# Optimization experiments

Hardware: AMD Instinct MI355X
Metric: run time of the kernel (lower is better)

Reference implementation:

```python
import jax, jax.numpy as jnp
import numpy as np
import math

B = 8; SEQ = 1000; C_IN = 32; D = 512; H = 8; DK = 64; DV = 64
DFF = 2048; NL = 4; ARY = 4; INNER = 5


def get_mask_np(seq_size, ary, inner):
    # full k-ary tree sizes (padded) and effective sizes per scale
    full = 1
    while full < seq_size:
        full *= ary
    all_size = [full]; effe = [seq_size]
    while all_size[-1] > 1:
        all_size.append(all_size[-1] // ary)
        effe.append(math.ceil(effe[-1] / ary))
    n = sum(all_size)
    allow = np.zeros((n, n), dtype=bool)
    w = inner // 2
    starts = np.concatenate([[0], np.cumsum(all_size)]).astype(int)
    # intra-scale local window
    for l, sz in enumerate(all_size):
        s = starts[l]
        for i in range(sz):
            lo = max(i - w, 0); hi = min(i + w + 1, sz)
            allow[s + i, s + lo:s + hi] = True
    # inter-scale parent<->children links
    for l in range(1, len(all_size)):
        s = starts[l]; ps = starts[l - 1]
        for i in range(all_size[l]):
            lo = ps + i * ary; hi = ps + (i + 1) * ary
            allow[s + i, lo:hi] = True
            allow[lo:hi, s + i] = True
    return allow, all_size, effe

ALLOW_NP, ALL_SIZE, EFFE_SIZE = get_mask_np(SEQ, ARY, INNER)
NTOT = sum(ALL_SIZE)   # 1365
DEPTH = len(ALL_SIZE)  # 6
OFFS = np.concatenate([[0], np.cumsum(ALL_SIZE)]).astype(int)


def sinusoid_pe(length, d):
    pos = np.arange(length)[:, None].astype(np.float64)
    i = np.arange(d)[None, :]
    ang = pos / np.power(10000.0, (2 * (i // 2)) / d)
    pe = np.zeros((length, d), np.float32)
    pe[:, 0::2] = np.sin(ang[:, 0::2]); pe[:, 1::2] = np.cos(ang[:, 1::2])
    return pe

PE_NP = sinusoid_pe(SEQ, D)


def layer_norm(x, s, b, eps=1e-5):
    m = x.mean(-1, keepdims=True)
    v = ((x - m) ** 2).mean(-1, keepdims=True)
    return (x - m) * jax.lax.rsqrt(v + eps) * s + b


def setup_inputs() -> dict:
    key = jax.random.key(0)
    ks = jax.random.split(key, 10)
    p = lambda k, shape, sc=0.02: jax.random.normal(k, shape, jnp.float32) * sc
    return {
        "x": jax.random.normal(ks[0], (B, SEQ, C_IN), jnp.float32),
        "conv_w": p(ks[1], (D, C_IN, 3), 0.05),
        "norm_s": jnp.ones((D,), jnp.float32), "norm_b": jnp.zeros((D,), jnp.float32),
        "wq": p(ks[2], (NL, D, H * DK)), "wk": p(ks[3], (NL, D, H * DK)),
        "wv": p(ks[4], (NL, D, H * DV)), "wo": p(ks[5], (NL, H * DV, D)),
        "ln1_s": jnp.ones((NL, D), jnp.float32), "ln1_b": jnp.zeros((NL, D), jnp.float32),
        "w1": p(ks[6], (NL, D, DFF)), "b1": jnp.zeros((NL, DFF), jnp.float32),
        "w2": p(ks[7], (NL, DFF, D)), "b2": jnp.zeros((NL, D), jnp.float32),
        "ln2_s": jnp.ones((NL, D), jnp.float32), "ln2_b": jnp.zeros((NL, D), jnp.float32),
    }


def reference(x, conv_w, norm_s, norm_b, wq, wk, wv, wo, ln1_s, ln1_b,
              w1, b1, w2, b2, ln2_s, ln2_b):
    allow = jnp.asarray(ALLOW_NP)        # [N,N] True = attend
    pe = jnp.asarray(PE_NP)              # [S,D]
    # --- DataEmbedding: conv1d(k=3, circular pad, no bias) + sinusoid PE ---
    xt = jnp.concatenate([x[:, -1:], x, x[:, :1]], axis=1)       # (B,S+2,C)
    emb = jax.lax.conv_general_dilated(
        xt, conv_w, (1,), 'VALID', dimension_numbers=('NWC', 'OIW', 'NWC'))
    emb = emb + pe[None]                                          # (B,S,D)
    # pad sequence to full-tree leaf count
    emb = jnp.pad(emb, ((0, 0), (0, ALL_SIZE[0] - SEQ), (0, 0)))  # (B,L0,D)
    # --- MaxPooling_Construct: pool by ary per level, concat, LayerNorm ---
    parts = [emb]
    cur = emb
    for lvl in range(DEPTH - 1):
        L = cur.shape[1]
        cur = cur.reshape(B, L // ARY, ARY, D).max(axis=2)
        parts.append(cur)
    seq = jnp.concatenate(parts, axis=1)                          # (B,N,D)
    seq = layer_norm(seq, norm_s, norm_b)
    # --- masked MHA encoder layers (post-norm) ---
    scale = 1.0 / math.sqrt(DK)
    neg = jnp.float32(-1e9)
    for l in range(NL):
        q = (seq @ wq[l]).reshape(B, NTOT, H, DK)
        k = (seq @ wk[l]).reshape(B, NTOT, H, DK)
        v = (seq @ wv[l]).reshape(B, NTOT, H, DV)
        scores = jnp.einsum('bnhd,bmhd->bhnm', q, k) * scale
        scores = jnp.where(allow[None, None], scores, neg)
        attn = jax.nn.softmax(scores, axis=-1)
        ctx = jnp.einsum('bhnm,bmhd->bnhd', attn, v).reshape(B, NTOT, H * DV)
        seq = layer_norm(seq + ctx @ wo[l], ln1_s[l], ln1_b[l])
        ff = jax.nn.gelu(seq @ w1[l] + b1[l], approximate=False) @ w2[l] + b2[l]
        seq = layer_norm(seq + ff, ln2_s[l], ln2_b[l])
    # --- keep only the effective (unpadded) prefix of each scale ---
    out = jnp.concatenate(
        [seq[:, OFFS[i]:OFFS[i] + EFFE_SIZE[i]] for i in range(DEPTH)], axis=1)
    return out  # (B, sum(effe)=1334, D)
```

## Files before the change

### kernel.cpp

```cpp
#include <hip/hip_runtime.h>
#include <cstdint>
#include <math.h>

#define DEV __device__ __forceinline__

static constexpr int BQ = 8, SEQN = 1000, CIN = 32, NH = 8;
static constexpr int NLAY = 4;
static constexpr int NTOT_C = 1365;
static constexpr int M_REAL = BQ * NTOT_C;
static constexpr int M_PAD  = 11008;

DEV float bf2f(unsigned short u){ return __uint_as_float(((unsigned)u) << 16); }
DEV unsigned short f2bf(float f){
  unsigned u = __float_as_uint(f);
  u += 0x7fffu + ((u >> 16) & 1u);
  return (unsigned short)(u >> 16);
}

typedef __bf16 bf16x8 __attribute__((ext_vector_type(8)));
typedef float  f32x4  __attribute__((ext_vector_type(4)));
typedef unsigned short u16x8 __attribute__((ext_vector_type(8)));

#define GLD_LDS16(gp, lp) __builtin_amdgcn_global_load_lds( \
    (const __attribute__((address_space(1))) void*)(gp), \
    (__attribute__((address_space(3))) void*)(lp), 16, 0, 0)

template<int N> DEV void waitcnt_vm(){
  asm volatile("s_waitcnt vmcnt(%0)" :: "i"(N) : "memory");
}
DEV void waitcnt_lgkm0(){ asm volatile("s_waitcnt lgkmcnt(0)" ::: "memory"); }
DEV void cfence(){ asm volatile("" ::: "memory"); }

DEV float gelu_f(float x){
  float z = 0.7978845608028654f * (x + 0.044715f * x * x * x);
  z = fminf(fmaxf(z, -10.f), 10.f);
  float e = __expf(2.f * z);
  float th = (e - 1.f) / (e + 1.f);
  return 0.5f * x * (1.f + th);
}

__global__ __launch_bounds__(256) void pe_kernel(float* __restrict__ pe)
{
  int idx = blockIdx.x * 256 + threadIdx.x;
  int d = idx & 511, s = idx >> 9;
  if (s >= SEQN) return;
  float e2 = (float)(d & ~1);
  float freq = exp2f(e2 * (-13.287712379549449f / 512.0f));
  float ang = (float)s * freq;
  pe[idx] = (d & 1) ? cosf(ang) : sinf(ang);
}

__global__ __launch_bounds__(256) void conv_kernel(const float* __restrict__ x,
    const float* __restrict__ w, const float* __restrict__ pe, float* __restrict__ seqf)
{
  __shared__ float ws_w[128 * 97];
  __shared__ __align__(16) float xs[66][32];
  int b = blockIdx.z, s0 = blockIdx.y * 64, d0 = blockIdx.x * 128;
  int tid = threadIdx.x;
  for (int i = tid; i < 128 * 96; i += 256){
    int r = i / 96, c = i - r * 96;
    ws_w[r * 97 + c] = w[(size_t)(d0 + r) * 96 + c];
  }
  for (int i = tid; i < 66 * 32; i += 256){
    int r = i >> 5, c = i & 31;
    int ss = s0 + r - 1;
    ss = (ss < 0) ? (ss + SEQN) : (ss >= SEQN ? ss - SEQN : ss);
    xs[r][c] = x[((size_t)b * SEQN + ss) * CIN + c];
  }
  __syncthreads();
  int dl = tid & 127, sh = tid >> 7;
  float wr[96];
  #pragma unroll
  for (int i = 0; i < 96; i++) wr[i] = ws_w[dl * 97 + i];
  int d = d0 + dl;
  for (int si = 0; si < 32; si++){
    int sl = sh * 32 + si;
    int s = s0 + sl;
    float acc = 0.f;
    #pragma unroll
    for (int kk = 0; kk < 3; kk++){
      const float* xr = xs[sl + kk];
      #pragma unroll
      for (int c = 0; c < 32; c++) acc += xr[c] * wr[c * 3 + kk];
    }
    float outv = (s < SEQN) ? acc + pe[(size_t)s * 512 + d] : 0.f;
    seqf[((size_t)b * NTOT_C + s) * 512 + d] = outv;
  }
}

__global__ __launch_bounds__(256) void pool_kernel(float* __restrict__ seqf,
    int inOff, int outOff, int outSz)
{
  int e = blockIdx.x * 256 + threadIdx.x;
  int d = e & 511;
  int r = e >> 9;
  int i = r % outSz;
  int b = r / outSz;
  const float* src = seqf + ((size_t)b * NTOT_C + inOff + 4 * i) * 512 + d;
  float m = fmaxf(fmaxf(src[0], src[512]), fmaxf(src[1024], src[1536]));
  seqf[((size_t)b * NTOT_C + outOff + i) * 512 + d] = m;
}

__global__ __launch_bounds__(256) void ln4_kernel(const float* __restrict__ xin,
    float* __restrict__ outf, unsigned short* __restrict__ outb,
    const float* __restrict__ sg, const float* __restrict__ bg, int M)
{
  int row = blockIdx.x * 4 + (threadIdx.x >> 6);
  int lane = threadIdx.x & 63;
  size_t base = (size_t)row * 512 + lane * 8;
  if (row >= M){
    f32x4 z4 = {0.f, 0.f, 0.f, 0.f};
    *reinterpret_cast<f32x4*>(outf + base) = z4;
    *reinterpret_cast<f32x4*>(outf + base + 4) = z4;
    u16x8 z8 = {0, 0, 0, 0, 0, 0, 0, 0};
    *reinterpret_cast<u16x8*>(outb + base) = z8;
    return;
  }
  f32x4 v0 = *reinterpret_cast<const f32x4*>(xin + base);
  f32x4 v1 = *reinterpret_cast<const f32x4*>(xin + base + 4);
  float sall = v0[0] + v0[1] + v0[2] + v0[3] + v1[0] + v1[1] + v1[2] + v1[3];
  #pragma unroll
  for (int o = 32; o; o >>= 1) sall += __shfl_xor(sall, o, 64);
  float mean = sall * (1.f / 512.f);
  float d[8];
  #pragma unroll
  for (int e = 0; e < 4; e++){ d[e] = v0[e] - mean; d[4 + e] = v1[e] - mean; }
  float sq = 0.f;
  #pragma unroll
  for (int e = 0; e < 8; e++) sq += d[e] * d[e];
  #pragma unroll
  for (int o = 32; o; o >>= 1) sq += __shfl_xor(sq, o, 64);
  float rstd = 1.f / sqrtf(sq * (1.f / 512.f) + 1e-5f);
  f32x4 s0 = *reinterpret_cast<const f32x4*>(sg + lane * 8);
  f32x4 s1 = *reinterpret_cast<const f32x4*>(sg + lane * 8 + 4);
  f32x4 g0 = *reinterpret_cast<const f32x4*>(bg + lane * 8);
  f32x4 g1 = *reinterpret_cast<const f32x4*>(bg + lane * 8 + 4);
  f32x4 y0, y1; u16x8 yb;
  #pragma unroll
  for (int e = 0; e < 4; e++){
    y0[e] = d[e] * rstd * s0[e] + g0[e];
    y1[e] = d[4 + e] * rstd * s1[e] + g1[e];
    yb[e] = f2bf(y0[e]); yb[4 + e] = f2bf(y1[e]);
  }
  *reinterpret_cast<f32x4*>(outf + base) = y0;
  *reinterpret_cast<f32x4*>(outf + base + 4) = y1;
  *reinterpret_cast<u16x8*>(outb + base) = yb;
}

__global__ __launch_bounds__(256) void wconv_all(
    const float* __restrict__ wq, const float* __restrict__ wk,
    const float* __restrict__ wv, const float* __restrict__ wo,
    const float* __restrict__ w1, const float* __restrict__ w2,
    unsigned short* __restrict__ qkvT, unsigned short* __restrict__ woT,
    unsigned short* __restrict__ w1T, unsigned short* __restrict__ w2T)
{
  __shared__ float tile[32][33];
  int bid = blockIdx.x;
  const float* wl; unsigned short* wtl; int N, K, n0, k0;
  if (bid < 4096){
    int part = bid >> 10, t = bid & 1023;
    int l = t >> 8, t2 = t & 255;
    k0 = (t2 >> 4) * 32; n0 = (t2 & 15) * 32;
    N = 512; K = 512;
    const float* s = (part == 0) ? wq : (part == 1) ? wk : (part == 2) ? wv : wo;
    wl = s + (size_t)l * 512 * 512;
    wtl = (part < 3) ? (qkvT + (size_t)l * 1536 * 512 + (size_t)part * 512 * 512)
                     : (woT + (size_t)l * 512 * 512);
  } else if (bid < 8192){
    int t = bid - 4096, l = t >> 10, t2 = t & 1023;
    k0 = (t2 >> 6) * 32; n0 = (t2 & 63) * 32;
    N = 2048; K = 512;
    wl = w1 + (size_t)l * 512 * 2048;
    wtl = w1T + (size_t)l * 2048 * 512;
  } else {
    int t = bid - 8192, l = t >> 10, t2 = t & 1023;
    k0 = (t2 >> 4) * 32; n0 = (t2 & 15) * 32;
    N = 512; K = 2048;
    wl = w2 + (size_t)l * 2048 * 512;
    wtl = w2T + (size_t)l * 512 * 2048;
  }
  int c = threadIdx.x & 31, r8 = threadIdx.x >> 5;
  #pragma unroll
  for (int p = 0; p < 4; p++){ int r = r8 + p * 8; tile[r][c] = wl[(size_t)(k0 + r) * N + n0 + c]; }
  __syncthreads();
  #pragma unroll
  for (int p = 0; p < 4; p++){ int r = r8 + p * 8; wtl[(size_t)(n0 + r) * K + k0 + c] = f2bf(tile[c][r]); }
}

template<int EPI, int BM, int BN>
__global__ __launch_bounds__(256) void gemm2_kernel(
    const unsigned short* __restrict__ A, const unsigned short* __restrict__ Wt,
    float* __restrict__ Cf, unsigned short* __restrict__ Cb,
    const float* __restrict__ bias, const float* __restrict__ Rf, int N, int K)
{
  constexpr int MF = BM / 32, NF = BN / 32;
  constexpr int LA = BM / 32, LB = BN / 32;
  __shared__ __align__(16) unsigned short Abuf[2][BM * 64];
  __shared__ __align__(16) unsigned short Bbuf[2][BN * 64];
  const int tid = threadIdx.x;
  const int wid = tid >> 6, lane = tid & 63;
  const int wm2 = wid >> 1, wn2 = wid & 1;
  const int r16 = lane & 15, g = lane >> 4;
  const int m0 = blockIdx.x * BM, n0 = blockIdx.y * BN;

  const int row0 = tid >> 3;
  const int scol = ((tid & 7) ^ (row0 & 7)) * 8;
  const unsigned short* gAs = A  + (size_t)(m0 + row0) * K + scol;
  const unsigned short* gBs = Wt + (size_t)(n0 + row0) * K + scol;

  const int swz0 = ((0 + g) ^ (r16 & 7)) * 8;
  const int swz1 = ((4 + g) ^ (r16 & 7)) * 8;
  const int arow = (wm2 * (BM / 2) + r16) * 64;
  const int brow = (wn2 * (BN / 2) + r16) * 64;

  const int nt = K >> 6;
  f32x4 acc[MF][NF] = {};

  auto STAGE_A = [&](int buf, int kt){
    #pragma unroll
    for (int q = 0; q < LA; q++)
      GLD_LDS16(gAs + kt * 64 + (size_t)q * 32 * K, &Abuf[buf][q * 2048 + tid * 8]);
  };
  auto STAGE_B = [&](int buf, int kt){
    #pragma unroll
    for (int q = 0; q < LB; q++)
      GLD_LDS16(gBs + kt * 64 + (size_t)q * 32 * K, &Bbuf[buf][q * 2048 + tid * 8]);
  };

  cfence();
  STAGE_A(0, 0); STAGE_B(0, 0);
  if (nt > 1){ STAGE_A(1, 1); waitcnt_vm<LA>(); }
  else        { waitcnt_vm<0>(); }
  __builtin_amdgcn_s_barrier();
  cfence();

  for (int t = 0; t < nt; t++){
    const int d = t & 1;
    const unsigned short* Ab = Abuf[d];
    const unsigned short* Bb = Bbuf[d];

    bf16x8 a0[MF], b0[NF];
    #pragma unroll
    for (int m = 0; m < MF; m++) a0[m] = *reinterpret_cast<const bf16x8*>(&Ab[arow + m * 1024 + swz0]);
    #pragma unroll
    for (int n = 0; n < NF; n++) b0[n] = *reinterpret_cast<const bf16x8*>(&Bb[brow + n * 1024 + swz0]);
    if (t + 1 < nt){ cfence(); STAGE_B(d ^ 1, t + 1); cfence(); }
    __builtin_amdgcn_s_setprio(1);
    #pragma unroll
    for (int m = 0; m < MF; m++)
      #pragma unroll
      for (int n = 0; n < NF; n++)
        acc[m][n] = __builtin_amdgcn_mfma_f32_16x16x32_bf16(a0[m], b0[n], acc[m][n], 0, 0, 0);
    __builtin_amdgcn_s_setprio(0);

    bf16x8 a1[MF], b1v[NF];
    #pragma unroll
    for (int m = 0; m < MF; m++) a1[m] = *reinterpret_cast<const bf16x8*>(&Ab[arow + m * 1024 + swz1]);
    #pragma unroll
    for (int n = 0; n < NF; n++) b1v[n] = *reinterpret_cast<const bf16x8*>(&Bb[brow + n * 1024 + swz1]);
    waitcnt_lgkm0();
    __builtin_amdgcn_s_barrier();
    cfence();
    if (t + 2 < nt){ STAGE_A(d, t + 2); cfence(); }
    __builtin_amdgcn_s_setprio(1);
    #pragma unroll
    for (int m = 0; m < MF; m++)
      #pragma unroll
      for (int n = 0; n < NF; n++)
        acc[m][n] = __builtin_amdgcn_mfma_f32_16x16x32_bf16(a1[m], b1v[n], acc[m][n], 0, 0, 0);
    __builtin_amdgcn_s_setprio(0);

    if (t + 1 < nt){
      if (t + 2 < nt) waitcnt_vm<LA>();
      else            waitcnt_vm<0>();
      __builtin_amdgcn_s_barrier();
      cfence();
    }
  }

  const int colBase = n0 + wn2 * (BN / 2) + r16;
  #pragma unroll
  for (int m = 0; m < MF; m++){
    int row = m0 + wm2 * (BM / 2) + m * 16 + g * 4;
    #pragma unroll
    for (int n = 0; n < NF; n++){
      int col = colBase + n * 16;
      float bsv = (EPI >= 2) ? bias[col] : 0.f;
      #pragma unroll
      for (int j = 0; j < 4; j++){
        float v = acc[m][n][j];
        if (EPI >= 2) v += bsv;
        if (EPI == 2) v = gelu_f(v);
        size_t off = (size_t)(row + j) * N + col;
        if (EPI == 0 || EPI == 3) Cf[off] = v + Rf[off];
        else                      Cb[off] = f2bf(v);
      }
    }
  }
}

__global__ __launch_bounds__(256) void attn_kernel(
    const unsigned short* __restrict__ qkv, unsigned short* __restrict__ ctx)
{
  int wid = blockIdx.x * 4 + (threadIdx.x >> 6);
  int lane = threadIdx.x & 63;
  int n = wid % NTOT_C;
  int b = wid / NTOT_C;

  int i, sz, of, cb, par;
  if (n < 1024){ i = n;        sz = 1024; of = 0;    cb = -1;            par = 1024 + (i >> 2); }
  else if (n < 1280){ i = n - 1024; sz = 256; of = 1024; cb = 0    + 4 * i; par = 1280 + (i >> 2); }
  else if (n < 1344){ i = n - 1280; sz = 64;  of = 1280; cb = 1024 + 4 * i; par = 1344 + (i >> 2); }
  else if (n < 1360){ i = n - 1344; sz = 16;  of = 1344; cb = 1280 + 4 * i; par = 1360 + (i >> 2); }
  else if (n < 1364){ i = n - 1360; sz = 4;   of = 1360; cb = 1344 + 4 * i; par = 1364; }
  else { i = 0; sz = 1; of = 1364; cb = 1360; par = -1; }

  int nb[10];
  #pragma unroll
  for (int s5 = 0; s5 < 5; s5++){ int pos = i - 2 + s5; nb[s5] = (pos >= 0 && pos < sz) ? of + pos : -1; }
  #pragma unroll
  for (int r = 0; r < 4; r++) nb[5 + r] = (cb >= 0) ? cb + r : -1;
  nb[9] = par;

  const unsigned short* rows = qkv + ((size_t)b * NTOT_C) * 1536;

  u16x8 qv = *reinterpret_cast<const u16x8*>(rows + (size_t)n * 1536 + lane * 8);
  float qf[8];
  #pragma unroll
  for (int e = 0; e < 8; e++) qf[e] = bf2f(qv[e]);

  float sc[10];
  #pragma unroll
  for (int j = 0; j < 10; j++){
    int id = nb[j] >= 0 ? nb[j] : n;
    u16x8 kv = *reinterpret_cast<const u16x8*>(rows + (size_t)id * 1536 + 512 + lane * 8);
    float p = 0.f;
    #pragma unroll
    for (int e = 0; e < 8; e++) p += qf[e] * bf2f(kv[e]);
    p += __shfl_xor(p, 1, 64);
    p += __shfl_xor(p, 2, 64);
    p += __shfl_xor(p, 4, 64);
    sc[j] = (nb[j] >= 0) ? p * 0.125f : -1e30f;
  }
  float mx = sc[0];
  #pragma unroll
  for (int j = 1; j < 10; j++) mx = fmaxf(mx, sc[j]);
  float den = 0.f;
  float wj[10];
  #pragma unroll
  for (int j = 0; j < 10; j++){
    wj[j] = (nb[j] >= 0) ? expf(sc[j] - mx) : 0.f;
    den += wj[j];
  }
  float rden = 1.f / den;
  float accv[8] = {};
  #pragma unroll
  for (int j = 0; j < 10; j++){
    int id = nb[j] >= 0 ? nb[j] : n;
    u16x8 vv = *reinterpret_cast<const u16x8*>(rows + (size_t)id * 1536 + 1024 + lane * 8);
    float w = wj[j];
    #pragma unroll
    for (int e = 0; e < 8; e++) accv[e] += w * bf2f(vv[e]);
  }
  u16x8 ov;
  #pragma unroll
  for (int e = 0; e < 8; e++) ov[e] = f2bf(accv[e] * rden);
  *reinterpret_cast<u16x8*>(ctx + ((size_t)b * NTOT_C + n) * 512 + lane * 8) = ov;
}

__global__ __launch_bounds__(256) void gather_kernel(const float* __restrict__ seqf,
    float* __restrict__ out)
{
  int e = blockIdx.x * 256 + threadIdx.x;
  int d = e & 511;
  int r = e >> 9;
  int j = r % 1334;
  int b = r / 1334;
  int src;
  if      (j < 1000) src = j;
  else if (j < 1250) src = j + 24;
  else if (j < 1313) src = j + 30;
  else if (j < 1333) src = j + 31;
  else               src = 1364;
  out[e] = seqf[((size_t)b * NTOT_C + src) * 512 + d];
}

extern "C" void kernel_launch(void* const* d_in, const int* in_sizes, int n_in,
                              void* d_out, int out_size, void* d_ws, size_t ws_size,
                              hipStream_t stream)
{
  const float* x      = (const float*)d_in[0];
  const float* conv_w = (const float*)d_in[1];
  const float* norm_s = (const float*)d_in[2];
  const float* norm_b = (const float*)d_in[3];
  const float* wq     = (const float*)d_in[4];
  const float* wk     = (const float*)d_in[5];
  const float* wv     = (const float*)d_in[6];
  const float* wo     = (const float*)d_in[7];
  const float* ln1_s  = (const float*)d_in[8];
  const float* ln1_b  = (const float*)d_in[9];
  const float* w1     = (const float*)d_in[10];
  const float* b1     = (const float*)d_in[11];
  const float* w2     = (const float*)d_in[12];
  const float* b2     = (const float*)d_in[13];
  const float* ln2_s  = (const float*)d_in[14];
  const float* ln2_b  = (const float*)d_in[15];
  float* out = (float*)d_out;

  char* ws = (char*)d_ws;
  size_t off = 0;
  auto alloc = [&](size_t bytes) -> char* {
    char* p = ws + off; off += (bytes + 255) & ~(size_t)255; return p;
  };
  unsigned short* qkvT = (unsigned short*)alloc((size_t)NLAY * 1536 * 512 * 2);
  unsigned short* woT  = (unsigned short*)alloc((size_t)NLAY * 512 * 512 * 2);
  unsigned short* w1T  = (unsigned short*)alloc((size_t)NLAY * 2048 * 512 * 2);
  unsigned short* w2T  = (unsigned short*)alloc((size_t)NLAY * 512 * 2048 * 2);
  float*          seqf = (float*)alloc((size_t)M_PAD * 512 * 4);
  unsigned short* seqb = (unsigned short*)alloc((size_t)M_PAD * 512 * 2);
  float*          buff = (float*)alloc((size_t)M_PAD * 512 * 4);
  unsigned short* qkvb = (unsigned short*)alloc((size_t)M_PAD * 1536 * 2);
  unsigned short* ctxb = (unsigned short*)alloc((size_t)M_PAD * 512 * 2);
  unsigned short* ffn1 = qkvb;
  float*          pe   = buff;

  wconv_all<<<12288, 256, 0, stream>>>(wq, wk, wv, wo, w1, w2, qkvT, woT, w1T, w2T);

  pe_kernel<<<(SEQN * 512) / 256, 256, 0, stream>>>(pe);
  conv_kernel<<<dim3(4,16,BQ), 256, 0, stream>>>(x, conv_w, pe, seqf);
  const int psz[6]  = {1024, 256, 64, 16, 4, 1};
  const int poff[6] = {0, 1024, 1280, 1344, 1360, 1364};
  for (int l = 0; l < 5; l++)
    pool_kernel<<<(BQ * psz[l+1] * 512) / 256, 256, 0, stream>>>(seqf, poff[l], poff[l+1], psz[l+1]);
  ln4_kernel<<<M_PAD / 4, 256, 0, stream>>>(seqf, seqf, seqb, norm_s, norm_b, M_REAL);

  for (int l = 0; l < NLAY; l++){
    gemm2_kernel<1,128,128><<<dim3(86,12),256,0,stream>>>(seqb, qkvT + (size_t)l*1536*512, nullptr, qkvb, nullptr, nullptr, 1536, 512);
    attn_kernel<<<(BQ * NTOT_C + 3) / 4, 256, 0, stream>>>(qkvb, ctxb);
    gemm2_kernel<0,64,128><<<dim3(172,4),256,0,stream>>>(ctxb, woT + (size_t)l*512*512, buff, nullptr, nullptr, seqf, 512, 512);
    ln4_kernel<<<M_PAD / 4, 256, 0, stream>>>(buff, seqf, seqb, ln1_s + l*512, ln1_b + l*512, M_REAL);
    gemm2_kernel<2,128,128><<<dim3(86,16),256,0,stream>>>(seqb, w1T + (size_t)l*2048*512, nullptr, ffn1, b1 + l*2048, nullptr, 2048, 512);
    gemm2_kernel<3,64,128><<<dim3(172,4),256,0,stream>>>(ffn1, w2T + (size_t)l*512*2048, buff, nullptr, b2 + l*512, seqf, 512, 2048);
    ln4_kernel<<<M_PAD / 4, 256, 0, stream>>>(buff, seqf, seqb, ln2_s + l*512, ln2_b + l*512, M_REAL);
  }

  gather_kernel<<<(BQ * 1334 * 512) / 256, 256, 0, stream>>>(seqf, out);
}
```

Measured before the change: 803.3 us.

## Keep residual stream in bf16 and move residual add into layernorm kernel

New measurement: 748.2 us. -6.9%, faster.

```diff
diff --git a/kernel.cpp b/kernel.cpp
--- a/kernel.cpp
+++ b/kernel.cpp
@@ -145,6 +145,59 @@
   *reinterpret_cast<f32x4*>(outf + base) = y0;
   *reinterpret_cast<f32x4*>(outf + base + 4) = y1;
   *reinterpret_cast<u16x8*>(outb + base) = yb;
+}
+
+template<bool WRITEF>
+__global__ __launch_bounds__(256) void lnres4_kernel(const unsigned short* __restrict__ cin,
+    float* __restrict__ outf, unsigned short* __restrict__ seqb,
+    const float* __restrict__ sg, const float* __restrict__ bg, int M)
+{
+  int row = blockIdx.x * 4 + (threadIdx.x >> 6);
+  int lane = threadIdx.x & 63;
+  size_t base = (size_t)row * 512 + lane * 8;
+  if (row >= M){
+    u16x8 z8 = {0, 0, 0, 0, 0, 0, 0, 0};
+    *reinterpret_cast<u16x8*>(seqb + base) = z8;
+    if (WRITEF){
+      f32x4 z4 = {0.f, 0.f, 0.f, 0.f};
+      *reinterpret_cast<f32x4*>(outf + base) = z4;
+      *reinterpret_cast<f32x4*>(outf + base + 4) = z4;
+    }
+    return;
+  }
+  u16x8 cv = *reinterpret_cast<const u16x8*>(cin + base);
+  u16x8 rv = *reinterpret_cast<const u16x8*>(seqb + base);
+  float v[8];
+  #pragma unroll
+  for (int e = 0; e < 8; e++) v[e] = bf2f(cv[e]) + bf2f(rv[e]);
+  float sall = 0.f;
+  #pragma unroll
+  for (int e = 0; e < 8; e++) sall += v[e];
+  #pragma unroll
+  for (int o = 32; o; o >>= 1) sall += __shfl_xor(sall, o, 64);
+  float mean = sall * (1.f / 512.f);
+  float sq = 0.f;
+  #pragma unroll
+  for (int e = 0; e < 8; e++){ v[e] -= mean; sq += v[e] * v[e]; }
+  #pragma unroll
+  for (int o = 32; o; o >>= 1) sq += __shfl_xor(sq, o, 64);
+  float rstd = 1.f / sqrtf(sq * (1.f / 512.f) + 1e-5f);
+  f32x4 s0 = *reinterpret_cast<const f32x4*>(sg + lane * 8);
+  f32x4 s1 = *reinterpret_cast<const f32x4*>(sg + lane * 8 + 4);
+  f32x4 g0 = *reinterpret_cast<const f32x4*>(bg + lane * 8);
+  f32x4 g1 = *reinterpret_cast<const f32x4*>(bg + lane * 8 + 4);
+  u16x8 yb; f32x4 y0, y1;
+  #pragma unroll
+  for (int e = 0; e < 4; e++){
+    y0[e] = v[e] * rstd * s0[e] + g0[e];
+    y1[e] = v[4 + e] * rstd * s1[e] + g1[e];
+    yb[e] = f2bf(y0[e]); yb[4 + e] = f2bf(y1[e]);
+  }
+  *reinterpret_cast<u16x8*>(seqb + base) = yb;
+  if (WRITEF){
+    *reinterpret_cast<f32x4*>(outf + base) = y0;
+    *reinterpret_cast<f32x4*>(outf + base + 4) = y1;
+  }
 }
 
 __global__ __launch_bounds__(256) void wconv_all(
@@ -190,8 +243,7 @@
 template<int EPI, int BM, int BN>
 __global__ __launch_bounds__(256) void gemm2_kernel(
     const unsigned short* __restrict__ A, const unsigned short* __restrict__ Wt,
-    float* __restrict__ Cf, unsigned short* __restrict__ Cb,
-    const float* __restrict__ bias, const float* __restrict__ Rf, int N, int K)
+    unsigned short* __restrict__ Cb, const float* __restrict__ bias, int N, int K)
 {
   constexpr int MF = BM / 32, NF = BN / 32;
   constexpr int LA = BM / 32, LB = BN / 32;
@@ -201,7 +253,7 @@
   const int wid = tid >> 6, lane = tid & 63;
   const int wm2 = wid >> 1, wn2 = wid & 1;
   const int r16 = lane & 15, g = lane >> 4;
-  const int m0 = blockIdx.x * BM, n0 = blockIdx.y * BN;
+  const int m0 = blockIdx.y * BM, n0 = blockIdx.x * BN;
 
   const int row0 = tid >> 3;
   const int scol = ((tid & 7) ^ (row0 & 7)) * 8;
@@ -291,9 +343,7 @@
         float v = acc[m][n][j];
         if (EPI >= 2) v += bsv;
         if (EPI == 2) v = gelu_f(v);
-        size_t off = (size_t)(row + j) * N + col;
-        if (EPI == 0 || EPI == 3) Cf[off] = v + Rf[off];
-        else                      Cb[off] = f2bf(v);
+        Cb[(size_t)(row + j) * N + col] = f2bf(v);
       }
     }
   }
@@ -423,6 +473,7 @@
   unsigned short* ctxb = (unsigned short*)alloc((size_t)M_PAD * 512 * 2);
   unsigned short* ffn1 = qkvb;
   float*          pe   = buff;
+  unsigned short* delta = (unsigned short*)buff;
 
   wconv_all<<<12288, 256, 0, stream>>>(wq, wk, wv, wo, w1, w2, qkvT, woT, w1T, w2T);
 
@@ -435,13 +486,16 @@
   ln4_kernel<<<M_PAD / 4, 256, 0, stream>>>(seqf, seqf, seqb, norm_s, norm_b, M_REAL);
 
   for (int l = 0; l < NLAY; l++){
-    gemm2_kernel<1,128,128><<<dim3(86,12),256,0,stream>>>(seqb, qkvT + (size_t)l*1536*512, nullptr, qkvb, nullptr, nullptr, 1536, 512);
+    gemm2_kernel<1,128,128><<<dim3(12,86),256,0,stream>>>(seqb, qkvT + (size_t)l*1536*512, qkvb, nullptr, 1536, 512);
     attn_kernel<<<(BQ * NTOT_C + 3) / 4, 256, 0, stream>>>(qkvb, ctxb);
-    gemm2_kernel<0,64,128><<<dim3(172,4),256,0,stream>>>(ctxb, woT + (size_t)l*512*512, buff, nullptr, nullptr, seqf, 512, 512);
-    ln4_kernel<<<M_PAD / 4, 256, 0, stream>>>(buff, seqf, seqb, ln1_s + l*512, ln1_b + l*512, M_REAL);
-    gemm2_kernel<2,128,128><<<dim3(86,16),256,0,stream>>>(seqb, w1T + (size_t)l*2048*512, nullptr, ffn1, b1 + l*2048, nullptr, 2048, 512);
-    gemm2_kernel<3,64,128><<<dim3(172,4),256,0,stream>>>(ffn1, w2T + (size_t)l*512*2048, buff, nullptr, b2 + l*512, seqf, 512, 2048);
-    ln4_kernel<<<M_PAD / 4, 256, 0, stream>>>(buff, seqf, seqb, ln2_s + l*512, ln2_b + l*512, M_REAL);
+    gemm2_kernel<1,64,128><<<dim3(4,172),256,0,stream>>>(ctxb, woT + (size_t)l*512*512, delta, nullptr, 512, 512);
+    lnres4_kernel<false><<<M_PAD / 4,256,0,stream>>>(delta, seqf, seqb, ln1_s + l*512, ln1_b + l*512, M_REAL);
+    gemm2_kernel<2,128,128><<<dim3(16,86),256,0,stream>>>(seqb, w1T + (size_t)l*2048*512, ffn1, b1 + l*2048, 2048, 512);
+    gemm2_kernel<4,64,128><<<dim3(4,172),256,0,stream>>>(ffn1, w2T + (size_t)l*512*2048, delta, b2 + l*512, 512, 2048);
+    if (l < NLAY - 1)
+      lnres4_kernel<false><<<M_PAD / 4,256,0,stream>>>(delta, seqf, seqb, ln2_s + l*512, ln2_b + l*512, M_REAL);
+    else
+      lnres4_kernel<true><<<M_PAD / 4,256,0,stream>>>(delta, seqf, seqb, ln2_s + l*512, ln2_b + l*512, M_REAL);
   }
 
   gather_kernel<<<(BQ * 1334 * 512) / 256, 256, 0, stream>>>(seqf, out);
```
